# Performance work log

Hardware: AMD Instinct MI355X
Metric: run time of the kernel (lower is better)

Reference implementation:

```python
import jax, jax.numpy as jnp
import numpy as np

B, T, C = 4, 2048, 1024
NH = 16
HD = C // NH


def setup_inputs() -> dict:
    key = jax.random.key(0)
    ks = jax.random.split(key, 5)
    s = 1.0 / np.sqrt(C)
    return {
        "x": jax.random.normal(ks[0], (B, T, C), dtype=jnp.float32),
        "W_qkv": jax.random.normal(ks[1], (C, 3 * C), dtype=jnp.float32) * s,
        "b_qkv": jnp.zeros((3 * C,), dtype=jnp.float32),
        "W_out": jax.random.normal(ks[2], (C, C), dtype=jnp.float32) * s,
        "b_out": jnp.zeros((C,), dtype=jnp.float32),
    }


def reference(x, W_qkv, b_qkv, W_out, b_out):
    Bx, Tx, Cx = x.shape
    qkv = x @ W_qkv + b_qkv                      # [B,T,3C]
    q, k, v = jnp.split(qkv, 3, axis=2)
    # [B,T,C] -> [B,NH,T,HD]
    q = q.reshape(Bx, Tx, NH, HD).transpose(0, 2, 1, 3)
    k = k.reshape(Bx, Tx, NH, HD).transpose(0, 2, 1, 3)
    v = v.reshape(Bx, Tx, NH, HD).transpose(0, 2, 1, 3)
    scale = 1.0 / np.sqrt(HD).astype(np.float32)
    attn = jnp.einsum('bhqd,bhkd->bhqk', q, k) * scale  # [B,NH,T,T]
    causal = jnp.tril(jnp.ones((Tx, Tx), dtype=bool))
    attn = jnp.where(causal[None, None], attn, jnp.float32(-jnp.inf))
    attn = jax.nn.softmax(attn, axis=-1)
    out = jnp.einsum('bhqk,bhkd->bhqd', attn, v)        # [B,NH,T,HD]
    out = out.transpose(0, 2, 1, 3).reshape(Bx, Tx, Cx)
    y = out @ W_out + b_out
    return (y, k, v)
```

## Files before the change

kernel.cpp:

```cpp
#include <hip/hip_runtime.h>
#include <cstdint>
#include <cstddef>

typedef __bf16 bf16x8 __attribute__((ext_vector_type(8)));
typedef __bf16 bf16x4 __attribute__((ext_vector_type(4)));
typedef float  f32x4  __attribute__((ext_vector_type(4)));

#define MFMA16(a, b, c) __builtin_amdgcn_mfma_f32_16x16x32_bf16((a), (b), (c), 0, 0, 0)

#define GLL16(gsrc, ldst)                                                              \
  __builtin_amdgcn_global_load_lds((__attribute__((address_space(1))) void*)(gsrc),    \
                                   (__attribute__((address_space(3))) void*)(ldst),    \
                                   16, 0, 0)

#define QSCALE 0.1803368801111204f


__global__ __launch_bounds__(256)
void cvt_f32_bf16(const float* __restrict__ in, __bf16* __restrict__ out, int n4)
{
    int i = blockIdx.x * 256 + threadIdx.x;
    if (i < n4) {
        float4 v = ((const float4*)in)[i];
        bf16x4 o;
        o[0] = (__bf16)v.x; o[1] = (__bf16)v.y; o[2] = (__bf16)v.z; o[3] = (__bf16)v.w;
        ((bf16x4*)out)[i] = o;
    }
}

__global__ __launch_bounds__(256)
void transpose_cvt(const float* __restrict__ in, __bf16* __restrict__ out, int K, int N)
{
    __shared__ __bf16 tile[32][33];
    const int n0 = blockIdx.x * 32, k0 = blockIdx.y * 32;
    const int tx = threadIdx.x, ty = threadIdx.y;
    #pragma unroll
    for (int i = 0; i < 4; ++i)
        tile[ty + i * 8][tx] = (__bf16)in[(size_t)(k0 + ty + i * 8) * N + n0 + tx];
    __syncthreads();
    #pragma unroll
    for (int i = 0; i < 4; ++i)
        out[(size_t)(n0 + ty + i * 8) * K + k0 + tx] = tile[tx][ty + i * 8];
}


__global__ __launch_bounds__(256)
void gemm_qkv(const __bf16* __restrict__ A, const __bf16* __restrict__ Bt,
              const float* __restrict__ bias,
              __bf16* __restrict__ qws, float* __restrict__ kout, float* __restrict__ vout,
              __bf16* __restrict__ kws, __bf16* __restrict__ vwst)
{
    constexpr int K = 1024;
    const int m0 = blockIdx.y * 128, n0 = blockIdx.x * 128;
    const int tid = threadIdx.x;
    const int wave = tid >> 6, lane = tid & 63;
    const int quad = lane >> 4, lr = lane & 15;
    const int wrow = (wave & 1) * 64, wcol = (wave >> 1) * 64;

    __shared__ __bf16 As[128 * 32];
    __shared__ __bf16 Bs[128 * 32];

    f32x4 acc[4][4];
    #pragma unroll
    for (int mi = 0; mi < 4; ++mi)
      #pragma unroll
      for (int ni = 0; ni < 4; ++ni)
        #pragma unroll
        for (int c = 0; c < 4; ++c) acc[mi][ni][c] = 0.f;

    const int u0 = tid, u1 = tid + 256;
    const int cg0 = ((u0 & 3) ^ ((u0 >> 3) & 3)) * 8;
    const int cg1 = ((u1 & 3) ^ ((u1 >> 3) & 3)) * 8;
    const __bf16* ga0 = A  + (size_t)(m0 + (u0 >> 2)) * K + cg0;
    const __bf16* ga1 = A  + (size_t)(m0 + (u1 >> 2)) * K + cg1;
    const __bf16* gb0 = Bt + (size_t)(n0 + (u0 >> 2)) * K + cg0;
    const __bf16* gb1 = Bt + (size_t)(n0 + (u1 >> 2)) * K + cg1;
    __bf16* la0 = As + u0 * 8;
    __bf16* la1 = As + u1 * 8;
    __bf16* lb0 = Bs + u0 * 8;
    __bf16* lb1 = Bs + u1 * 8;

    const int sw = (quad ^ ((lr >> 1) & 3)) * 8;

    for (int kt = 0; kt < K; kt += 32) {
        __syncthreads();
        GLL16(ga0 + kt, la0);
        GLL16(ga1 + kt, la1);
        GLL16(gb0 + kt, lb0);
        GLL16(gb1 + kt, lb1);
        __syncthreads();
        bf16x8 af[4], bfv[4];
        #pragma unroll
        for (int mi = 0; mi < 4; ++mi)
            af[mi] = *(const bf16x8*)&As[(wrow + mi * 16 + lr) * 32 + sw];
        #pragma unroll
        for (int ni = 0; ni < 4; ++ni)
            bfv[ni] = *(const bf16x8*)&Bs[(wcol + ni * 16 + lr) * 32 + sw];
        #pragma unroll
        for (int mi = 0; mi < 4; ++mi)
          #pragma unroll
          for (int ni = 0; ni < 4; ++ni)
            acc[mi][ni] = MFMA16(af[mi], bfv[ni], acc[mi][ni]);
    }

    const int sec = n0 >> 10;
    #pragma unroll
    for (int ni = 0; ni < 4; ++ni) {
        const int gn = n0 + wcol + ni * 16 + lr;
        const float bv = bias[gn];
        const int cn = gn & 1023, hh = cn >> 6, dd = cn & 63;
        #pragma unroll
        for (int mi = 0; mi < 4; ++mi) {
            const int gm0 = m0 + wrow + mi * 16 + quad * 4;
            const int b = gm0 >> 11, t0 = gm0 & 2047;
            const size_t tb = ((size_t)b * 16 + hh) * 2048;
            if (sec == 0) {
                #pragma unroll
                for (int r = 0; r < 4; ++r)
                    qws[(tb + t0 + r) * 64 + dd] = (__bf16)((acc[mi][ni][r] + bv) * QSCALE);
            } else if (sec == 1) {
                #pragma unroll
                for (int r = 0; r < 4; ++r) {
                    const float val = acc[mi][ni][r] + bv;
                    kout[(tb + t0 + r) * 64 + dd] = val;
                    kws [(tb + t0 + r) * 64 + dd] = (__bf16)val;
                }
            } else {
                bf16x4 pk;
                #pragma unroll
                for (int r = 0; r < 4; ++r) {
                    const float val = acc[mi][ni][r] + bv;
                    vout[(tb + t0 + r) * 64 + dd] = val;
                    pk[r] = (__bf16)val;
                }
                *(bf16x4*)&vwst[(((size_t)b * 16 + hh) * 64 + dd) * 2048 + t0] = pk;
            }
        }
    }
}

__global__ __launch_bounds__(256)
void gemm_out(const __bf16* __restrict__ A, const __bf16* __restrict__ Bt,
              const float* __restrict__ bias, float* __restrict__ y)
{
    constexpr int K = 1024;
    const int m0 = blockIdx.y * 128, n0 = blockIdx.x * 128;
    const int tid = threadIdx.x;
    const int wave = tid >> 6, lane = tid & 63;
    const int quad = lane >> 4, lr = lane & 15;
    const int wrow = (wave & 1) * 64, wcol = (wave >> 1) * 64;

    __shared__ __bf16 As[128 * 32];
    __shared__ __bf16 Bs[128 * 32];

    f32x4 acc[4][4];
    #pragma unroll
    for (int mi = 0; mi < 4; ++mi)
      #pragma unroll
      for (int ni = 0; ni < 4; ++ni)
        #pragma unroll
        for (int c = 0; c < 4; ++c) acc[mi][ni][c] = 0.f;

    const int u0 = tid, u1 = tid + 256;
    const int cg0 = ((u0 & 3) ^ ((u0 >> 3) & 3)) * 8;
    const int cg1 = ((u1 & 3) ^ ((u1 >> 3) & 3)) * 8;
    const __bf16* ga0 = A  + (size_t)(m0 + (u0 >> 2)) * K + cg0;
    const __bf16* ga1 = A  + (size_t)(m0 + (u1 >> 2)) * K + cg1;
    const __bf16* gb0 = Bt + (size_t)(n0 + (u0 >> 2)) * K + cg0;
    const __bf16* gb1 = Bt + (size_t)(n0 + (u1 >> 2)) * K + cg1;
    __bf16* la0 = As + u0 * 8;
    __bf16* la1 = As + u1 * 8;
    __bf16* lb0 = Bs + u0 * 8;
    __bf16* lb1 = Bs + u1 * 8;

    const int sw = (quad ^ ((lr >> 1) & 3)) * 8;

    for (int kt = 0; kt < K; kt += 32) {
        __syncthreads();
        GLL16(ga0 + kt, la0);
        GLL16(ga1 + kt, la1);
        GLL16(gb0 + kt, lb0);
        GLL16(gb1 + kt, lb1);
        __syncthreads();
        bf16x8 af[4], bfv[4];
        #pragma unroll
        for (int mi = 0; mi < 4; ++mi)
            af[mi] = *(const bf16x8*)&As[(wrow + mi * 16 + lr) * 32 + sw];
        #pragma unroll
        for (int ni = 0; ni < 4; ++ni)
            bfv[ni] = *(const bf16x8*)&Bs[(wcol + ni * 16 + lr) * 32 + sw];
        #pragma unroll
        for (int mi = 0; mi < 4; ++mi)
          #pragma unroll
          for (int ni = 0; ni < 4; ++ni)
            acc[mi][ni] = MFMA16(af[mi], bfv[ni], acc[mi][ni]);
    }

    #pragma unroll
    for (int ni = 0; ni < 4; ++ni) {
        const int gn = n0 + wcol + ni * 16 + lr;
        const float bv = bias[gn];
        #pragma unroll
        for (int mi = 0; mi < 4; ++mi) {
            #pragma unroll
            for (int r = 0; r < 4; ++r) {
                const int gm = m0 + wrow + mi * 16 + quad * 4 + r;
                y[(size_t)gm * 1024 + gn] = acc[mi][ni][r] + bv;
            }
        }
    }
}


__global__ __launch_bounds__(256, 2)
void attn_fused(const __bf16* __restrict__ qws, const __bf16* __restrict__ kws,
                const __bf16* __restrict__ vwst, __bf16* __restrict__ attnws)
{
    const int bh = blockIdx.y;
    const int tid = threadIdx.x;
    const int wave = tid >> 6, lane = tid & 63;
    const int quad = lane >> 4, lr = lane & 15;

    const int jq[2] = { (int)blockIdx.x, 15 - (int)blockIdx.x };
    const int nt[2] = { 2 * (jq[0] + 1), 2 * (jq[1] + 1) };
    const int ntB = nt[1];

    __shared__ __bf16 Ks [2][2][64][32];
    __shared__ __bf16 Vts[2][2][64][32];
    __shared__ __bf16 Ps [4][32][72];

    bf16x8 aq[2][2][2];
    #pragma unroll
    for (int h = 0; h < 2; ++h)
      #pragma unroll
      for (int mi = 0; mi < 2; ++mi) {
        const __bf16* qb = qws + ((size_t)bh * 2048 + jq[h] * 128 + wave * 32 + mi * 16 + lr) * 64 + quad * 8;
        aq[h][mi][0] = *(const bf16x8*)qb;
        aq[h][mi][1] = *(const bf16x8*)(qb + 32);
      }

    bf16x8 ones;
    #pragma unroll
    for (int j = 0; j < 8; ++j) ones[j] = (__bf16)1.0f;

    float m_i[2][2][4];
    f32x4 o_acc[2][2][4], l_acc[2][2];
    #pragma unroll
    for (int h = 0; h < 2; ++h)
      #pragma unroll
      for (int mi = 0; mi < 2; ++mi) {
        #pragma unroll
        for (int r = 0; r < 4; ++r) { m_i[h][mi][r] = -1e30f; l_acc[h][mi][r] = 0.f; }
        #pragma unroll
        for (int n = 0; n < 4; ++n)
          #pragma unroll
          for (int r = 0; r < 4; ++r) o_acc[h][mi][n][r] = 0.f;
      }

    const int srow = tid >> 2;
    const int scg  = ((tid & 3) ^ ((tid >> 3) & 3)) * 8;
    const __bf16* kb = kws  + ((size_t)bh * 2048 + srow) * 64 + scg;
    const __bf16* vb = vwst + ((size_t)bh * 64 + srow) * 2048 + scg;
    char* lk = (char*)Ks  + tid * 16;
    char* lv = (char*)Vts + tid * 16;

    const int sw = (quad ^ ((lr >> 1) & 3)) * 8;

    GLL16(kb,      lk);
    GLL16(kb + 32, lk + 4096);
    GLL16(vb,      lv);
    GLL16(vb + 32, lv + 4096);

    for (int jt = 0; jt < ntB; ++jt) {
        const int cur = jt & 1;
        if (jt + 1 < ntB) {
            const int nb = (jt + 1) & 1;
            GLL16(kb + (size_t)(jt + 1) * 4096,      lk + nb * 8192);
            GLL16(kb + (size_t)(jt + 1) * 4096 + 32, lk + nb * 8192 + 4096);
            GLL16(vb + (jt + 1) * 64,                lv + nb * 8192);
            GLL16(vb + (jt + 1) * 64 + 32,           lv + nb * 8192 + 4096);
            asm volatile("s_waitcnt vmcnt(4)" ::: "memory");
        } else {
            asm volatile("s_waitcnt vmcnt(0)" ::: "memory");
        }
        asm volatile("s_barrier" ::: "memory");

        bf16x8 bk[4][2];
        #pragma unroll
        for (int ni = 0; ni < 4; ++ni) {
            bk[ni][0] = *(const bf16x8*)&Ks[cur][0][ni * 16 + lr][sw];
            bk[ni][1] = *(const bf16x8*)&Ks[cur][1][ni * 16 + lr][sw];
        }

        #pragma unroll
        for (int h = 0; h < 2; ++h) {
            if (jt < nt[h]) {
                f32x4 sacc[2][4];
                #pragma unroll
                for (int mi = 0; mi < 2; ++mi)
                  #pragma unroll
                  for (int ni = 0; ni < 4; ++ni)
                    #pragma unroll
                    for (int c = 0; c < 4; ++c) sacc[mi][ni][c] = 0.f;
                #pragma unroll
                for (int ni = 0; ni < 4; ++ni)
                  #pragma unroll
                  for (int mi = 0; mi < 2; ++mi) {
                    sacc[mi][ni] = MFMA16(aq[h][mi][0], bk[ni][0], sacc[mi][ni]);
                    sacc[mi][ni] = MFMA16(aq[h][mi][1], bk[ni][1], sacc[mi][ni]);
                  }

                if (jt >= nt[h] - 2) {
                    const int c0 = jt * 64 + lr;
                    #pragma unroll
                    for (int mi = 0; mi < 2; ++mi) {
                        const int t0 = jq[h] * 128 + wave * 32 + mi * 16 + quad * 4;
                        #pragma unroll
                        for (int ni = 0; ni < 4; ++ni)
                          #pragma unroll
                          for (int r = 0; r < 4; ++r)
                            if (c0 + ni * 16 > t0 + r) sacc[mi][ni][r] = -1e30f;
                    }
                }

                #pragma unroll
                for (int mi = 0; mi < 2; ++mi) {
                    float alpha[4];
                    #pragma unroll
                    for (int r = 0; r < 4; ++r) {
                        float mx = fmaxf(fmaxf(sacc[mi][0][r], sacc[mi][1][r]),
                                         fmaxf(sacc[mi][2][r], sacc[mi][3][r]));
                        mx = fmaxf(mx, __shfl_xor(mx, 1));
                        mx = fmaxf(mx, __shfl_xor(mx, 2));
                        mx = fmaxf(mx, __shfl_xor(mx, 4));
                        mx = fmaxf(mx, __shfl_xor(mx, 8));
                        const float mnew = fmaxf(m_i[h][mi][r], mx);
                        alpha[r] = __builtin_amdgcn_exp2f(m_i[h][mi][r] - mnew);
                        m_i[h][mi][r] = mnew;
                        #pragma unroll
                        for (int ni = 0; ni < 4; ++ni) {
                            const float p = __builtin_amdgcn_exp2f(sacc[mi][ni][r] - mnew);
                            Ps[wave][mi * 16 + quad * 4 + r][ni * 16 + lr] = (__bf16)p;
                        }
                    }
                    #pragma unroll
                    for (int n = 0; n < 4; ++n)
                      #pragma unroll
                      for (int r = 0; r < 4; ++r) o_acc[h][mi][n][r] *= alpha[r];
                    #pragma unroll
                    for (int r = 0; r < 4; ++r) l_acc[h][mi][r] *= alpha[r];
                }

                asm volatile("s_waitcnt lgkmcnt(0)" ::: "memory");

                bf16x8 bv[4][2];
                #pragma unroll
                for (int n = 0; n < 4; ++n) {
                    bv[n][0] = *(const bf16x8*)&Vts[cur][0][n * 16 + lr][sw];
                    bv[n][1] = *(const bf16x8*)&Vts[cur][1][n * 16 + lr][sw];
                }
                #pragma unroll
                for (int mi = 0; mi < 2; ++mi) {
                    bf16x8 ap0 = *(const bf16x8*)&Ps[wave][mi * 16 + lr][quad * 8];
                    bf16x8 ap1 = *(const bf16x8*)&Ps[wave][mi * 16 + lr][32 + quad * 8];
                    l_acc[h][mi] = MFMA16(ap0, ones, l_acc[h][mi]);
                    l_acc[h][mi] = MFMA16(ap1, ones, l_acc[h][mi]);
                    #pragma unroll
                    for (int n = 0; n < 4; ++n) {
                        o_acc[h][mi][n] = MFMA16(ap0, bv[n][0], o_acc[h][mi][n]);
                        o_acc[h][mi][n] = MFMA16(ap1, bv[n][1], o_acc[h][mi][n]);
                    }
                }
            }
        }

        asm volatile("s_waitcnt lgkmcnt(0)" ::: "memory");
        asm volatile("s_barrier" ::: "memory");
    }

    const int b = bh >> 4, h16 = bh & 15;
    #pragma unroll
    for (int h = 0; h < 2; ++h)
      #pragma unroll
      for (int mi = 0; mi < 2; ++mi)
        #pragma unroll
        for (int r = 0; r < 4; ++r) {
            const int t = jq[h] * 128 + wave * 32 + mi * 16 + quad * 4 + r;
            const float inv = 1.f / l_acc[h][mi][r];
            #pragma unroll
            for (int n = 0; n < 4; ++n)
                attnws[(((size_t)b * 2048 + t) * 16 + h16) * 64 + n * 16 + lr] =
                    (__bf16)(o_acc[h][mi][n][r] * inv);
        }
}


extern "C" void kernel_launch(void* const* d_in, const int* in_sizes, int n_in,
                              void* d_out, int out_size, void* d_ws, size_t ws_size,
                              hipStream_t stream)
{
    (void)in_sizes; (void)n_in; (void)out_size; (void)ws_size;

    const float* x    = (const float*)d_in[0];
    const float* Wqkv = (const float*)d_in[1];
    const float* bqkv = (const float*)d_in[2];
    const float* Wout = (const float*)d_in[3];
    const float* bout = (const float*)d_in[4];

    float* y    = (float*)d_out;
    float* kout = y + 8388608;
    float* vout = kout + 8388608;

    char* ws = (char*)d_ws;
    __bf16* xb    = (__bf16*)(ws);
    __bf16* wqkvt = (__bf16*)(ws + (16u << 20));
    __bf16* woutt = (__bf16*)(ws + (22u << 20));
    __bf16* qws   = (__bf16*)(ws + (24u << 20));
    __bf16* kws   = (__bf16*)(ws + (40u << 20));
    __bf16* vwst  = (__bf16*)(ws + (56u << 20));
    __bf16* attnw = (__bf16*)(ws + (72u << 20));

    cvt_f32_bf16<<<8192, 256, 0, stream>>>(x, xb, 2097152);
    transpose_cvt<<<dim3(96, 32), dim3(32, 8), 0, stream>>>(Wqkv, wqkvt, 1024, 3072);
    transpose_cvt<<<dim3(32, 32), dim3(32, 8), 0, stream>>>(Wout, woutt, 1024, 1024);
    gemm_qkv<<<dim3(24, 64), 256, 0, stream>>>(xb, wqkvt, bqkv, qws, kout, vout, kws, vwst);
    attn_fused<<<dim3(8, 64), 256, 0, stream>>>(qws, kws, vwst, attnw);
    gemm_out<<<dim3(8, 64), 256, 0, stream>>>(attnw, woutt, bout, y);
}
```

Before: 343.4 us.

## Serialize attention query halves, skip fully-masked tiles, split out V transpose

The attention kernel now handles its two paired query blocks one after another, with a single continuous K/V prefetch stream, instead of running both inside one loop. This halves the live accumulator state, which allows raising launch bounds to 3 blocks per SM. Waves whose last key tile lies entirely above the diagonal now skip it, and P is written to LDS as packed bf16x4 stores. The strided transposed V write moves out of the QKV GEMM into a separate vtrans kernel that reads the fp32 V output back, at the cost of an extra launch and extra memory traffic.

```diff
diff --git a/kernel.cpp b/kernel.cpp
--- a/kernel.cpp
+++ b/kernel.cpp
@@ -45,10 +45,48 @@
 
 
 __global__ __launch_bounds__(256)
+void vtrans(const float* __restrict__ vout, __bf16* __restrict__ vwst)
+{
+    const int bh = blockIdx.y;
+    const int t0 = blockIdx.x * 64;
+    const int tid = threadIdx.x;
+
+    __shared__ __bf16 VT[64][68];
+
+    const int tr = tid >> 4;
+    const int dc = (tid & 15) * 4;
+
+    float4 vals[4];
+    #pragma unroll
+    for (int i = 0; i < 4; ++i)
+        vals[i] = *(const float4*)&vout[((size_t)bh * 2048 + t0 + tr + 16 * i) * 64 + dc];
+
+    #pragma unroll
+    for (int j = 0; j < 4; ++j) {
+        bf16x4 pk;
+        pk[0] = (__bf16)(&vals[0].x)[j];
+        pk[1] = (__bf16)(&vals[1].x)[j];
+        pk[2] = (__bf16)(&vals[2].x)[j];
+        pk[3] = (__bf16)(&vals[3].x)[j];
+        *(bf16x4*)&VT[dc + j][4 * tr] = pk;
+    }
+    __syncthreads();
+
+    #pragma unroll
+    for (int k = 0; k < 2; ++k) {
+        const int c = tid + 256 * k;
+        const int d = c >> 3, off = (c & 7) * 8;
+        bf16x8 v = *(const bf16x8*)&VT[d][off];
+        *(bf16x8*)&vwst[((size_t)bh * 64 + d) * 2048 + t0 + off] = v;
+    }
+}
+
+
+__global__ __launch_bounds__(256)
 void gemm_qkv(const __bf16* __restrict__ A, const __bf16* __restrict__ Bt,
               const float* __restrict__ bias,
               __bf16* __restrict__ qws, float* __restrict__ kout, float* __restrict__ vout,
-              __bf16* __restrict__ kws, __bf16* __restrict__ vwst)
+              __bf16* __restrict__ kws)
 {
     constexpr int K = 1024;
     const int m0 = blockIdx.y * 128, n0 = blockIdx.x * 128;
@@ -126,14 +164,9 @@
                     kws [(tb + t0 + r) * 64 + dd] = (__bf16)val;
                 }
             } else {
-                bf16x4 pk;
-                #pragma unroll
-                for (int r = 0; r < 4; ++r) {
-                    const float val = acc[mi][ni][r] + bv;
-                    vout[(tb + t0 + r) * 64 + dd] = val;
-                    pk[r] = (__bf16)val;
-                }
-                *(bf16x4*)&vwst[(((size_t)b * 16 + hh) * 64 + dd) * 2048 + t0] = pk;
+                #pragma unroll
+                for (int r = 0; r < 4; ++r)
+                    vout[(tb + t0 + r) * 64 + dd] = acc[mi][ni][r] + bv;
             }
         }
     }
@@ -212,7 +245,7 @@
 }
 
 
-__global__ __launch_bounds__(256, 2)
+__global__ __launch_bounds__(256, 3)
 void attn_fused(const __bf16* __restrict__ qws, const __bf16* __restrict__ kws,
                 const __bf16* __restrict__ vwst, __bf16* __restrict__ attnws)
 {
@@ -221,41 +254,14 @@
     const int wave = tid >> 6, lane = tid & 63;
     const int quad = lane >> 4, lr = lane & 15;
 
-    const int jq[2] = { (int)blockIdx.x, 15 - (int)blockIdx.x };
-    const int nt[2] = { 2 * (jq[0] + 1), 2 * (jq[1] + 1) };
-    const int ntB = nt[1];
+    const int jqp[2] = { (int)blockIdx.x, 15 - (int)blockIdx.x };
+    const int ntp[2] = { 2 * (jqp[0] + 1), 2 * (jqp[1] + 1) };
+    const int nt0 = ntp[0];
+    const int ntot = ntp[0] + ntp[1];
 
     __shared__ __bf16 Ks [2][2][64][32];
     __shared__ __bf16 Vts[2][2][64][32];
     __shared__ __bf16 Ps [4][32][72];
-
-    bf16x8 aq[2][2][2];
-    #pragma unroll
-    for (int h = 0; h < 2; ++h)
-      #pragma unroll
-      for (int mi = 0; mi < 2; ++mi) {
-        const __bf16* qb = qws + ((size_t)bh * 2048 + jq[h] * 128 + wave * 32 + mi * 16 + lr) * 64 + quad * 8;
-        aq[h][mi][0] = *(const bf16x8*)qb;
-        aq[h][mi][1] = *(const bf16x8*)(qb + 32);
-      }
-
-    bf16x8 ones;
-    #pragma unroll
-    for (int j = 0; j < 8; ++j) ones[j] = (__bf16)1.0f;
-
-    float m_i[2][2][4];
-    f32x4 o_acc[2][2][4], l_acc[2][2];
-    #pragma unroll
-    for (int h = 0; h < 2; ++h)
-      #pragma unroll
-      for (int mi = 0; mi < 2; ++mi) {
-        #pragma unroll
-        for (int r = 0; r < 4; ++r) { m_i[h][mi][r] = -1e30f; l_acc[h][mi][r] = 0.f; }
-        #pragma unroll
-        for (int n = 0; n < 4; ++n)
-          #pragma unroll
-          for (int r = 0; r < 4; ++r) o_acc[h][mi][n][r] = 0.f;
-      }
 
     const int srow = tid >> 2;
     const int scg  = ((tid & 3) ^ ((tid >> 3) & 3)) * 8;
@@ -266,35 +272,65 @@
 
     const int sw = (quad ^ ((lr >> 1) & 3)) * 8;
 
+    bf16x8 ones;
+    #pragma unroll
+    for (int j = 0; j < 8; ++j) ones[j] = (__bf16)1.0f;
+
+    const int b = bh >> 4, h16 = bh & 15;
+
     GLL16(kb,      lk);
     GLL16(kb + 32, lk + 4096);
     GLL16(vb,      lv);
     GLL16(vb + 32, lv + 4096);
 
-    for (int jt = 0; jt < ntB; ++jt) {
-        const int cur = jt & 1;
-        if (jt + 1 < ntB) {
-            const int nb = (jt + 1) & 1;
-            GLL16(kb + (size_t)(jt + 1) * 4096,      lk + nb * 8192);
-            GLL16(kb + (size_t)(jt + 1) * 4096 + 32, lk + nb * 8192 + 4096);
-            GLL16(vb + (jt + 1) * 64,                lv + nb * 8192);
-            GLL16(vb + (jt + 1) * 64 + 32,           lv + nb * 8192 + 4096);
-            asm volatile("s_waitcnt vmcnt(4)" ::: "memory");
-        } else {
-            asm volatile("s_waitcnt vmcnt(0)" ::: "memory");
+    int pos = 0;
+    for (int h = 0; h < 2; ++h) {
+        const int jq = jqp[h];
+        const int NT = ntp[h];
+
+        bf16x8 aq[2][2];
+        #pragma unroll
+        for (int mi = 0; mi < 2; ++mi) {
+            const __bf16* qb = qws + ((size_t)bh * 2048 + jq * 128 + wave * 32 + mi * 16 + lr) * 64 + quad * 8;
+            aq[mi][0] = *(const bf16x8*)qb;
+            aq[mi][1] = *(const bf16x8*)(qb + 32);
         }
-        asm volatile("s_barrier" ::: "memory");
-
-        bf16x8 bk[4][2];
-        #pragma unroll
-        for (int ni = 0; ni < 4; ++ni) {
-            bk[ni][0] = *(const bf16x8*)&Ks[cur][0][ni * 16 + lr][sw];
-            bk[ni][1] = *(const bf16x8*)&Ks[cur][1][ni * 16 + lr][sw];
+
+        float m_i[2][4];
+        f32x4 o_acc[2][4], l_acc[2];
+        #pragma unroll
+        for (int mi = 0; mi < 2; ++mi) {
+            #pragma unroll
+            for (int r = 0; r < 4; ++r) { m_i[mi][r] = -1e30f; l_acc[mi][r] = 0.f; }
+            #pragma unroll
+            for (int n = 0; n < 4; ++n)
+                #pragma unroll
+                for (int r = 0; r < 4; ++r) o_acc[mi][n][r] = 0.f;
         }
 
-        #pragma unroll
-        for (int h = 0; h < 2; ++h) {
-            if (jt < nt[h]) {
+        for (int jt = 0; jt < NT; ++jt, ++pos) {
+            const int cur = pos & 1;
+            if (pos + 1 < ntot) {
+                const int nj = (pos + 1 < nt0) ? pos + 1 : pos + 1 - nt0;
+                const int nb = (pos + 1) & 1;
+                GLL16(kb + (size_t)nj * 4096,      lk + nb * 8192);
+                GLL16(kb + (size_t)nj * 4096 + 32, lk + nb * 8192 + 4096);
+                GLL16(vb + nj * 64,                lv + nb * 8192);
+                GLL16(vb + nj * 64 + 32,           lv + nb * 8192 + 4096);
+                asm volatile("s_waitcnt vmcnt(4)" ::: "memory");
+            } else {
+                asm volatile("s_waitcnt vmcnt(0)" ::: "memory");
+            }
+            asm volatile("s_barrier" ::: "memory");
+
+            const bool lastTile = (jt == NT - 1);
+            if (!(lastTile && wave < 2)) {
+                bf16x8 bk[4][2];
+                #pragma unroll
+                for (int ni = 0; ni < 4; ++ni) {
+                    bk[ni][0] = *(const bf16x8*)&Ks[cur][0][ni * 16 + lr][sw];
+                    bk[ni][1] = *(const bf16x8*)&Ks[cur][1][ni * 16 + lr][sw];
+                }
                 f32x4 sacc[2][4];
                 #pragma unroll
                 for (int mi = 0; mi < 2; ++mi)
@@ -306,15 +342,16 @@
                 for (int ni = 0; ni < 4; ++ni)
                   #pragma unroll
                   for (int mi = 0; mi < 2; ++mi) {
-                    sacc[mi][ni] = MFMA16(aq[h][mi][0], bk[ni][0], sacc[mi][ni]);
-                    sacc[mi][ni] = MFMA16(aq[h][mi][1], bk[ni][1], sacc[mi][ni]);
+                    sacc[mi][ni] = MFMA16(aq[mi][0], bk[ni][0], sacc[mi][ni]);
+                    sacc[mi][ni] = MFMA16(aq[mi][1], bk[ni][1], sacc[mi][ni]);
                   }
 
-                if (jt >= nt[h] - 2) {
+                const bool needMask = (jt == NT - 2 && wave < 2) || (lastTile && wave >= 2);
+                if (needMask) {
                     const int c0 = jt * 64 + lr;
                     #pragma unroll
                     for (int mi = 0; mi < 2; ++mi) {
-                        const int t0 = jq[h] * 128 + wave * 32 + mi * 16 + quad * 4;
+                        const int t0 = jq * 128 + wave * 32 + mi * 16 + quad * 4;
                         #pragma unroll
                         for (int ni = 0; ni < 4; ++ni)
                           #pragma unroll
@@ -334,21 +371,21 @@
                         mx = fmaxf(mx, __shfl_xor(mx, 2));
                         mx = fmaxf(mx, __shfl_xor(mx, 4));
                         mx = fmaxf(mx, __shfl_xor(mx, 8));
-                        const float mnew = fmaxf(m_i[h][mi][r], mx);
-                        alpha[r] = __builtin_amdgcn_exp2f(m_i[h][mi][r] - mnew);
-                        m_i[h][mi][r] = mnew;
+                        const float mnew = fmaxf(m_i[mi][r], mx);
+                        alpha[r] = __builtin_amdgcn_exp2f(m_i[mi][r] - mnew);
+                        m_i[mi][r] = mnew;
+                        bf16x4 pp;
                         #pragma unroll
-                        for (int ni = 0; ni < 4; ++ni) {
-                            const float p = __builtin_amdgcn_exp2f(sacc[mi][ni][r] - mnew);
-                            Ps[wave][mi * 16 + quad * 4 + r][ni * 16 + lr] = (__bf16)p;
-                        }
+                        for (int ni = 0; ni < 4; ++ni)
+                            pp[ni] = (__bf16)__builtin_amdgcn_exp2f(sacc[mi][ni][r] - mnew);
+                        *(bf16x4*)&Ps[wave][mi * 16 + quad * 4 + r][4 * lr] = pp;
                     }
                     #pragma unroll
                     for (int n = 0; n < 4; ++n)
                       #pragma unroll
-                      for (int r = 0; r < 4; ++r) o_acc[h][mi][n][r] *= alpha[r];
-                    #pragma unroll
-                    for (int r = 0; r < 4; ++r) l_acc[h][mi][r] *= alpha[r];
+                      for (int r = 0; r < 4; ++r) o_acc[mi][n][r] *= alpha[r];
+                    #pragma unroll
+                    for (int r = 0; r < 4; ++r) l_acc[mi][r] *= alpha[r];
                 }
 
                 asm volatile("s_waitcnt lgkmcnt(0)" ::: "memory");
@@ -363,35 +400,32 @@
                 for (int mi = 0; mi < 2; ++mi) {
                     bf16x8 ap0 = *(const bf16x8*)&Ps[wave][mi * 16 + lr][quad * 8];
                     bf16x8 ap1 = *(const bf16x8*)&Ps[wave][mi * 16 + lr][32 + quad * 8];
-                    l_acc[h][mi] = MFMA16(ap0, ones, l_acc[h][mi]);
-                    l_acc[h][mi] = MFMA16(ap1, ones, l_acc[h][mi]);
+                    l_acc[mi] = MFMA16(ap0, ones, l_acc[mi]);
+                    l_acc[mi] = MFMA16(ap1, ones, l_acc[mi]);
                     #pragma unroll
                     for (int n = 0; n < 4; ++n) {
-                        o_acc[h][mi][n] = MFMA16(ap0, bv[n][0], o_acc[h][mi][n]);
-                        o_acc[h][mi][n] = MFMA16(ap1, bv[n][1], o_acc[h][mi][n]);
+                        o_acc[mi][n] = MFMA16(ap0, bv[n][0], o_acc[mi][n]);
+                        o_acc[mi][n] = MFMA16(ap1, bv[n][1], o_acc[mi][n]);
                     }
                 }
             }
+
+            asm volatile("s_waitcnt lgkmcnt(0)" ::: "memory");
+            asm volatile("s_barrier" ::: "memory");
         }
 
-        asm volatile("s_waitcnt lgkmcnt(0)" ::: "memory");
-        asm volatile("s_barrier" ::: "memory");
-    }
-
-    const int b = bh >> 4, h16 = bh & 15;
-    #pragma unroll
-    for (int h = 0; h < 2; ++h)
-      #pragma unroll
-      for (int mi = 0; mi < 2; ++mi)
-        #pragma unroll
-        for (int r = 0; r < 4; ++r) {
-            const int t = jq[h] * 128 + wave * 32 + mi * 16 + quad * 4 + r;
-            const float inv = 1.f / l_acc[h][mi][r];
+        #pragma unroll
+        for (int mi = 0; mi < 2; ++mi)
+          #pragma unroll
+          for (int r = 0; r < 4; ++r) {
+            const int t = jq * 128 + wave * 32 + mi * 16 + quad * 4 + r;
+            const float inv = 1.f / l_acc[mi][r];
             #pragma unroll
             for (int n = 0; n < 4; ++n)
                 attnws[(((size_t)b * 2048 + t) * 16 + h16) * 64 + n * 16 + lr] =
-                    (__bf16)(o_acc[h][mi][n][r] * inv);
-        }
+                    (__bf16)(o_acc[mi][n][r] * inv);
+          }
+    }
 }
 
 
@@ -423,7 +457,8 @@
     cvt_f32_bf16<<<8192, 256, 0, stream>>>(x, xb, 2097152);
     transpose_cvt<<<dim3(96, 32), dim3(32, 8), 0, stream>>>(Wqkv, wqkvt, 1024, 3072);
     transpose_cvt<<<dim3(32, 32), dim3(32, 8), 0, stream>>>(Wout, woutt, 1024, 1024);
-    gemm_qkv<<<dim3(24, 64), 256, 0, stream>>>(xb, wqkvt, bqkv, qws, kout, vout, kws, vwst);
+    gemm_qkv<<<dim3(24, 64), 256, 0, stream>>>(xb, wqkvt, bqkv, qws, kout, vout, kws);
+    vtrans<<<dim3(32, 64), 256, 0, stream>>>(vout, vwst);
     attn_fused<<<dim3(8, 64), 256, 0, stream>>>(qws, kws, vwst, attnw);
     gemm_out<<<dim3(8, 64), 256, 0, stream>>>(attnw, woutt, bout, y);
 }
```

New measurement: 337.2 us. About the same (-1.8%).
